# Kernel optimization log

Measured on AMD Instinct MI355X. Metric: run time of the kernel, lower is better.

Reference implementation:

```python
import jax, jax.numpy as jnp
import numpy as np

D = 1024  # d_model

def setup_inputs() -> dict:
    key = jax.random.key(0)
    ks = jax.random.split(key, 12)
    s = 1.0 / np.sqrt(D)  # torch Linear default init scale
    inp = {
        "q": jax.random.normal(ks[0], (4, 4096, D), dtype=jnp.float32),
        "k": jax.random.normal(ks[1], (4, 4096, D), dtype=jnp.float32),
        "v": jax.random.normal(ks[2], (4, 4096, D), dtype=jnp.float32),
        "Wq": jax.random.uniform(ks[3], (D, D), jnp.float32, -s, s),
        "bq": jax.random.uniform(ks[4], (D,), jnp.float32, -s, s),
        "Wk": jax.random.uniform(ks[5], (D, D), jnp.float32, -s, s),
        "bk": jax.random.uniform(ks[6], (D,), jnp.float32, -s, s),
        "Wv": jax.random.uniform(ks[7], (D, D), jnp.float32, -s, s),
        "bv": jax.random.uniform(ks[8], (D,), jnp.float32, -s, s),
        "Wo": jax.random.uniform(ks[9], (D, D), jnp.float32, -s, s),
        "bo": jax.random.uniform(ks[10], (D,), jnp.float32, -s, s),
    }
    return inp

def reference(q, k, v, Wq, bq, Wk, bk, Wv, bv, Wo, bo):
    # phi feature map: exp(-x^2 / 2)
    phi = lambda x: jnp.exp(-0.5 * x * x)
    Q = phi(q @ Wq.T + bq)            # [B, N, D]
    K = phi(k @ Wk.T + bk)            # [B, N, D]
    V = v @ Wv.T + bv                 # [B, N, D]
    # linear attention: aggregate K^T V once, then contract with Q
    KV = jnp.einsum('bnd,bnl->bdl', K, V)                 # [B, D, D]
    Z = 1.0 / (jnp.einsum('bnd,bd->bn', Q, K.sum(axis=1)) + 1e-6)  # [B, N]
    out = jnp.einsum('bnd,bdl->bnl', Q, KV) * Z[..., None]         # [B, N, D]
    return out @ Wo.T + bo
```

## Files before the change

kernel.cpp:

```cpp
#include <hip/hip_runtime.h>

typedef unsigned short u16;
typedef unsigned int u32;
typedef unsigned long long u64;

typedef __attribute__((ext_vector_type(8))) short short8;
typedef __attribute__((ext_vector_type(4))) float floatx4;

__device__ __forceinline__ float b2f(u16 h) {
  u32 u = ((u32)h) << 16;
  return __builtin_bit_cast(float, u);
}
__device__ __forceinline__ u16 f2b(float f) {
  u32 u = __builtin_bit_cast(u32, f);
  u32 r = 0x7FFFu + ((u >> 16) & 1u);
  return (u16)((u + r) >> 16);
}

__device__ __forceinline__ void gl_lds16(const void* g, void* l) {
  __builtin_amdgcn_global_load_lds(
      (__attribute__((address_space(1))) void*)(u64)g,
      (__attribute__((address_space(3))) void*)(u32)(u64)l, 16, 0, 0);
}

enum { EPI_PHI_BIAS = 0, EPI_BIAS = 1, EPI_NONE = 2,
       EPI_ZBIAS_F32 = 3 };

template<int EPI, bool TRANS_OUT>
__global__ __launch_bounds__(512, 2)
void gemm_bt256(const u16* __restrict__ Ap, const u16* __restrict__ Bp0,
                const float* __restrict__ bias, const float* __restrict__ Zall,
                void* __restrict__ Cp,
                int M, int N, int K, int ldA, int ldB, int ldC,
                long sAb, long sBb, long sCb, long sZb, int abmask, int kshift)
{
  constexpr int TSTRIDE = 65536;
  constexpr int BOFF    = 32768;
  __shared__ char smem[2 * TSTRIDE];

  const int tid  = threadIdx.x;
  const int lane = tid & 63;
  const int wave = tid >> 6;
  const int wm = wave >> 2, wn = wave & 3;
  const int fl = lane & 15;
  const int q  = lane >> 4;
  const int r4 = q * 4;
  const int bm0 = blockIdx.x * 256, bn0 = blockIdx.y * 256;
  const int bz = blockIdx.z;
  const int abz = bz & abmask;
  const int kbase = (bz >> kshift) * K;

  const u16* Ah = Ap  + (size_t)abz * sAb + kbase;
  const u16* Bh = Bp0 + (size_t)abz * sBb + kbase;

  const u16* gA[4]; const u16* gB[4]; int sL[4];
  #pragma unroll
  for (int n = 0; n < 4; ++n) {
    int j = n * 512 + tid;
    int R = j >> 3, c = (j & 7) ^ (R & 7);
    gA[n] = Ah + (size_t)(bm0 + R) * ldA + c * 8;
    gB[n] = Bh + (size_t)(bn0 + R) * ldB + c * 8;
    sL[n] = (n * 512 + wave * 64) * 16;
  }

  int aoff[8], boff[4];
  #pragma unroll
  for (int i = 0; i < 8; ++i) {
    int ra = wm * 128 + i * 16 + fl;
    aoff[i] = ra * 128 + ((q ^ (ra & 7)) * 16);
  }
  #pragma unroll
  for (int i = 0; i < 4; ++i) {
    int rb = wn * 64 + i * 16 + fl;
    boff[i] = rb * 128 + ((q ^ (rb & 7)) * 16);
  }

  floatx4 zero = {0.f, 0.f, 0.f, 0.f};
  floatx4 acc[8][4];
  #pragma unroll
  for (int i = 0; i < 8; ++i)
    #pragma unroll
    for (int j = 0; j < 4; ++j) acc[i][j] = zero;

  auto stage = [&](int t, char* base) {
    int k0 = t * 64;
    #pragma unroll
    for (int n = 0; n < 4; ++n) gl_lds16(gA[n] + k0, base + sL[n]);
    #pragma unroll
    for (int n = 0; n < 4; ++n) gl_lds16(gB[n] + k0, base + BOFF + sL[n]);
  };

  auto kstep = [&](const char* bufc, int xo) {
    short8 bF[4], aF[8];
    #pragma unroll
    for (int i = 0; i < 4; ++i) bF[i] = *(const short8*)(bufc + BOFF + (boff[i] ^ xo));
    #pragma unroll
    for (int i = 0; i < 8; ++i) aF[i] = *(const short8*)(bufc + (aoff[i] ^ xo));
    __builtin_amdgcn_s_setprio(1);
    #pragma unroll
    for (int mi = 0; mi < 8; ++mi)
      #pragma unroll
      for (int ni = 0; ni < 4; ++ni)
        acc[mi][ni] = __builtin_amdgcn_mfma_f32_16x16x32_bf16(
            aF[mi], bF[ni], acc[mi][ni], 0, 0, 0);
    __builtin_amdgcn_s_setprio(0);
  };

  const int NT = K >> 6;
  stage(0, smem);
  asm volatile("s_waitcnt vmcnt(0)\ns_barrier" ::: "memory");
  int cur = 0;
  for (int t = 0; t < NT; ++t) {
    if (t + 1 < NT) stage(t + 1, smem + (cur ^ TSTRIDE));
    const char* bufc = smem + cur;
    kstep(bufc, 0);
    kstep(bufc, 64);
    if (t + 1 < NT)
      asm volatile("s_waitcnt vmcnt(0) lgkmcnt(0)\ns_barrier" ::: "memory");
    cur ^= TSTRIDE;
  }

  if constexpr (!TRANS_OUT) {
    #pragma unroll
    for (int mi = 0; mi < 8; ++mi) {
      #pragma unroll
      for (int ni = 0; ni < 4; ++ni) {
        int col = bn0 + wn * 64 + ni * 16 + fl;
        #pragma unroll
        for (int r = 0; r < 4; ++r) {
          int row = bm0 + wm * 128 + mi * 16 + r4 + r;
          float vv = acc[mi][ni][r];
          if constexpr (EPI == EPI_PHI_BIAS) {
            vv += bias[col];
            vv = __expf(-0.5f * vv * vv);
          }
          if constexpr (EPI == EPI_ZBIAS_F32)
            vv = vv * Zall[(size_t)abz * sZb + row] + bias[col];
          if constexpr (EPI == EPI_ZBIAS_F32)
            ((float*)Cp)[(size_t)bz * sCb + (size_t)row * ldC + col] = vv;
          else
            ((u16*)Cp)[(size_t)bz * sCb + (size_t)row * ldC + col] = f2b(vv);
        }
      }
    }
  } else {
    u16* sT = (u16*)smem;
    #pragma unroll
    for (int p = 0; p < 2; ++p) {
      __syncthreads();
      if ((wn >> 1) == p) {
        #pragma unroll
        for (int mi = 0; mi < 8; ++mi) {
          #pragma unroll
          for (int ni = 0; ni < 4; ++ni) {
            int colL = wn * 64 + ni * 16 + fl;
            int row0 = wm * 128 + mi * 16 + r4;
            float bcol = bias[bn0 + colL];
            ushort4 h;
            #pragma unroll
            for (int r = 0; r < 4; ++r) {
              float vv = acc[mi][ni][r] + bcol;
              if constexpr (EPI == EPI_PHI_BIAS) vv = __expf(-0.5f * vv * vv);
              ((u16*)&h)[r] = f2b(vv);
            }
            *(ushort4*)(sT + (colL - p * 128) * 264 + row0) = h;
          }
        }
      }
      __syncthreads();
      #pragma unroll
      for (int i = 0; i < 8; ++i) {
        int c = tid + i * 512;
        int dloc = c >> 5, t8 = (c & 31) * 8;
        int4 vv = *(const int4*)(sT + dloc * 264 + t8);
        int gd = bn0 + p * 128 + dloc;
        int gt = bm0 + t8;
        int batch = gt >> 12, tt = gt & 4095;
        *(int4*)((u16*)Cp + ((size_t)batch * N + gd) * 4096 + tt) = vv;
      }
    }
  }
}

__global__ __launch_bounds__(256)
void fcvt(const float* __restrict__ src, u16* __restrict__ dst) {
  size_t i = ((size_t)blockIdx.x * 256 + threadIdx.x) * 8;
  float4 a = *(const float4*)(src + i);
  float4 b = *(const float4*)(src + i + 4);
  union { ushort4 h[2]; int4 v; } o;
  o.h[0].x = f2b(a.x); o.h[0].y = f2b(a.y); o.h[0].z = f2b(a.z); o.h[0].w = f2b(a.w);
  o.h[1].x = f2b(b.x); o.h[1].y = f2b(b.y); o.h[1].z = f2b(b.z); o.h[1].w = f2b(b.w);
  *(int4*)(dst + i) = o.v;
}

__global__ __launch_bounds__(256)
void wconv(const float* __restrict__ w0, const float* __restrict__ w1,
           const float* __restrict__ w2, const float* __restrict__ w3,
           u16* __restrict__ dst) {
  unsigned e = blockIdx.x * 256 + threadIdx.x;
  int mat = e >> 18;
  size_t off = (size_t)(e & 262143) * 4;
  const float* src = mat == 0 ? w0 : mat == 1 ? w1 : mat == 2 ? w2 : w3;
  float4 v = *(const float4*)(src + off);
  ushort4 h;
  h.x = f2b(v.x); h.y = f2b(v.y); h.z = f2b(v.z); h.w = f2b(v.w);
  *(ushort4*)(dst + (size_t)mat * 1048576 + off) = h;
}

__global__ __launch_bounds__(256)
void reduce4(const u16* __restrict__ P, u16* __restrict__ out) {
  size_t i = ((size_t)blockIdx.x * 256 + threadIdx.x) * 8;
  int4 a = *(const int4*)(P + i);
  int4 b = *(const int4*)(P + i + 4194304);
  int4 c = *(const int4*)(P + i + 8388608);
  int4 d = *(const int4*)(P + i + 12582912);
  const u16* ha = (const u16*)&a; const u16* hb = (const u16*)&b;
  const u16* hc = (const u16*)&c; const u16* hd = (const u16*)&d;
  ushort4 o0, o1;
  #pragma unroll
  for (int j = 0; j < 8; ++j) {
    float s = b2f(ha[j]) + b2f(hb[j]) + b2f(hc[j]) + b2f(hd[j]);
    ((u16*)(j < 4 ? &o0 : &o1))[j & 3] = f2b(s);
  }
  *(ushort4*)(out + i) = o0;
  *(ushort4*)(out + i + 4) = o1;
}

__global__ __launch_bounds__(256)
void ksum_rows(const u16* __restrict__ KT, float* __restrict__ Ksum) {
  int lane = threadIdx.x & 63;
  int row = blockIdx.x * 4 + (threadIdx.x >> 6);
  const u16* p = KT + (size_t)row * 4096;
  float s = 0.f;
  #pragma unroll
  for (int i = 0; i < 8; ++i) {
    int4 d = *(const int4*)(p + i * 512 + lane * 8);
    const u16* h = (const u16*)&d;
    #pragma unroll
    for (int j = 0; j < 8; ++j) s += b2f(h[j]);
  }
  #pragma unroll
  for (int off = 32; off; off >>= 1) s += __shfl_xor(s, off, 64);
  if (lane == 0) Ksum[row] = s;
}

__global__ __launch_bounds__(256)
void zden(const u16* __restrict__ Qb, const float* __restrict__ Ksum,
          float* __restrict__ Z) {
  int lane = threadIdx.x & 63;
  int t = blockIdx.x * 4 + (threadIdx.x >> 6);
  const u16* qp = Qb + (size_t)t * 1024;
  const float* ks = Ksum + (size_t)(t >> 12) * 1024;
  float s = 0.f;
  #pragma unroll
  for (int i = 0; i < 2; ++i) {
    int idx = i * 512 + lane * 8;
    int4 d = *(const int4*)(qp + idx);
    const u16* h = (const u16*)&d;
    float4 k0 = *(const float4*)(ks + idx);
    float4 k1 = *(const float4*)(ks + idx + 4);
    s += b2f(h[0]) * k0.x + b2f(h[1]) * k0.y + b2f(h[2]) * k0.z + b2f(h[3]) * k0.w
       + b2f(h[4]) * k1.x + b2f(h[5]) * k1.y + b2f(h[6]) * k1.z + b2f(h[7]) * k1.w;
  }
  #pragma unroll
  for (int off = 32; off; off >>= 1) s += __shfl_xor(s, off, 64);
  if (lane == 0) Z[t] = 1.0f / (s + 1e-6f);
}

extern "C" void kernel_launch(void* const* d_in, const int* in_sizes, int n_in,
                              void* d_out, int out_size, void* d_ws, size_t ws_size,
                              hipStream_t stream) {
  const float* q  = (const float*)d_in[0];
  const float* k  = (const float*)d_in[1];
  const float* v  = (const float*)d_in[2];
  const float* Wq = (const float*)d_in[3];
  const float* bq = (const float*)d_in[4];
  const float* Wk = (const float*)d_in[5];
  const float* bk = (const float*)d_in[6];
  const float* Wv = (const float*)d_in[7];
  const float* bv = (const float*)d_in[8];
  const float* Wo = (const float*)d_in[9];
  const float* bo = (const float*)d_in[10];
  float* out = (float*)d_out;

  u16* Wqb = (u16*)d_ws;
  u16* Wkb = Wqb + 1048576;
  u16* Wvb = Wkb + 1048576;
  u16* Wob = Wvb + 1048576;
  u16* Qb  = Wob + 1048576;
  u16* KT  = Qb  + 16777216;
  u16* VT  = KT  + 16777216;
  u16* KVr = VT  + 16777216;
  float* Ksum = (float*)(KVr + 4194304);
  float* Z    = Ksum + 4096;
  u16* kb16 = Qb;
  u16* vb16 = Qb;
  u16* Pkv  = Qb;
  u16* Pg   = VT;
  u16* Gp   = KT;
  u16* qb16 = VT;

  wconv<<<4096, 256, 0, stream>>>(Wq, Wk, Wv, Wo, Wqb);
  fcvt<<<8192, 256, 0, stream>>>(k, kb16);

  dim3 gp(64, 4, 1);
  gemm_bt256<EPI_PHI_BIAS, true><<<gp, 512, 0, stream>>>(
      kb16, Wkb, bk, nullptr, KT, 16384, 1024, 1024, 1024, 1024, 0,
      0, 0, 0, 0, 0, 2);
  ksum_rows<<<1024, 256, 0, stream>>>(KT, Ksum);

  fcvt<<<8192, 256, 0, stream>>>(v, vb16);
  gemm_bt256<EPI_BIAS, true><<<gp, 512, 0, stream>>>(
      vb16, Wvb, bv, nullptr, VT, 16384, 1024, 1024, 1024, 1024, 0,
      0, 0, 0, 0, 0, 2);

  dim3 g2(4, 4, 16);
  gemm_bt256<EPI_NONE, false><<<g2, 512, 0, stream>>>(
      KT, VT, nullptr, nullptr, Pkv, 1024, 1024, 1024, 4096, 4096, 1024,
      4194304L, 4194304L, 1048576L, 0, 3, 2);
  reduce4<<<2048, 256, 0, stream>>>(Pkv, KVr);

  dim3 gg(4, 4, 16);
  gemm_bt256<EPI_NONE, false><<<gg, 512, 0, stream>>>(
      Wob, KVr, nullptr, nullptr, Pg, 1024, 1024, 256, 1024, 1024, 1024,
      0L, 1048576L, 1048576L, 0, 3, 2);
  reduce4<<<2048, 256, 0, stream>>>(Pg, Gp);

  fcvt<<<8192, 256, 0, stream>>>(q, qb16);
  gemm_bt256<EPI_PHI_BIAS, false><<<gp, 512, 0, stream>>>(
      qb16, Wqb, bq, nullptr, Qb, 16384, 1024, 1024, 1024, 1024, 1024,
      0, 0, 0, 0, 0, 2);
  zden<<<4096, 256, 0, stream>>>(Qb, Ksum, Z);

  dim3 gf(16, 4, 4);
  gemm_bt256<EPI_ZBIAS_F32, false><<<gf, 512, 0, stream>>>(
      Qb, Gp, bo, Z, out, 4096, 1024, 1024, 1024, 1024, 1024,
      4194304L, 1048576L, 4194304L, 4096L, 3, 2);
}
```

Before: 301.2 us.

## Split GEMM k-loop into four quadrant phases interleaving LDS reads, prefetch, and MFMA

```diff
diff --git a/kernel.cpp b/kernel.cpp
--- a/kernel.cpp
+++ b/kernel.cpp
@@ -90,32 +90,101 @@
     for (int n = 0; n < 4; ++n) gl_lds16(gB[n] + k0, base + BOFF + sL[n]);
   };
 
-  auto kstep = [&](const char* bufc, int xo) {
-    short8 bF[4], aF[8];
-    #pragma unroll
-    for (int i = 0; i < 4; ++i) bF[i] = *(const short8*)(bufc + BOFF + (boff[i] ^ xo));
-    #pragma unroll
-    for (int i = 0; i < 8; ++i) aF[i] = *(const short8*)(bufc + (aoff[i] ^ xo));
-    __builtin_amdgcn_s_setprio(1);
-    #pragma unroll
-    for (int mi = 0; mi < 8; ++mi)
-      #pragma unroll
-      for (int ni = 0; ni < 4; ++ni)
-        acc[mi][ni] = __builtin_amdgcn_mfma_f32_16x16x32_bf16(
-            aF[mi], bF[ni], acc[mi][ni], 0, 0, 0);
-    __builtin_amdgcn_s_setprio(0);
-  };
-
   const int NT = K >> 6;
   stage(0, smem);
   asm volatile("s_waitcnt vmcnt(0)\ns_barrier" ::: "memory");
   int cur = 0;
   for (int t = 0; t < NT; ++t) {
-    if (t + 1 < NT) stage(t + 1, smem + (cur ^ TSTRIDE));
+    const bool pf = t + 1 < NT;
     const char* bufc = smem + cur;
-    kstep(bufc, 0);
-    kstep(bufc, 64);
-    if (t + 1 < NT)
+    char* stb = smem + (cur ^ TSTRIDE);
+    const int k1 = (t + 1) * 64;
+    short8 aL[8], aH[8], b01[4], b23[4];
+
+    #pragma unroll
+    for (int i = 0; i < 4; ++i) {
+      aL[2 * i]     = *(const short8*)(bufc + aoff[i]);
+      aL[2 * i + 1] = *(const short8*)(bufc + (aoff[i] ^ 64));
+    }
+    #pragma unroll
+    for (int i = 0; i < 2; ++i) {
+      b01[2 * i]     = *(const short8*)(bufc + BOFF + boff[i]);
+      b01[2 * i + 1] = *(const short8*)(bufc + BOFF + (boff[i] ^ 64));
+    }
+    if (pf) {
+      #pragma unroll
+      for (int n = 0; n < 4; ++n) gl_lds16(gA[n] + k1, stb + sL[n]);
+    }
+    __builtin_amdgcn_s_barrier();
+    asm volatile("s_waitcnt lgkmcnt(0)" ::: "memory");
+    __builtin_amdgcn_sched_barrier(0);
+    __builtin_amdgcn_s_setprio(1);
+    #pragma unroll
+    for (int kk = 0; kk < 2; ++kk)
+      #pragma unroll
+      for (int mi = 0; mi < 4; ++mi)
+        #pragma unroll
+        for (int ni = 0; ni < 2; ++ni)
+          acc[mi][ni] = __builtin_amdgcn_mfma_f32_16x16x32_bf16(
+              aL[2 * mi + kk], b01[2 * ni + kk], acc[mi][ni], 0, 0, 0);
+    __builtin_amdgcn_s_setprio(0);
+    __builtin_amdgcn_s_barrier();
+
+    #pragma unroll
+    for (int i = 0; i < 2; ++i) {
+      b23[2 * i]     = *(const short8*)(bufc + BOFF + boff[i + 2]);
+      b23[2 * i + 1] = *(const short8*)(bufc + BOFF + (boff[i + 2] ^ 64));
+    }
+    if (pf) {
+      #pragma unroll
+      for (int n = 0; n < 4; ++n) gl_lds16(gB[n] + k1, stb + BOFF + sL[n]);
+    }
+    __builtin_amdgcn_s_barrier();
+    asm volatile("s_waitcnt lgkmcnt(0)" ::: "memory");
+    __builtin_amdgcn_sched_barrier(0);
+    __builtin_amdgcn_s_setprio(1);
+    #pragma unroll
+    for (int kk = 0; kk < 2; ++kk)
+      #pragma unroll
+      for (int mi = 0; mi < 4; ++mi)
+        #pragma unroll
+        for (int ni = 0; ni < 2; ++ni)
+          acc[mi][ni + 2] = __builtin_amdgcn_mfma_f32_16x16x32_bf16(
+              aL[2 * mi + kk], b23[2 * ni + kk], acc[mi][ni + 2], 0, 0, 0);
+    __builtin_amdgcn_s_setprio(0);
+    __builtin_amdgcn_s_barrier();
+
+    #pragma unroll
+    for (int i = 0; i < 4; ++i) {
+      aH[2 * i]     = *(const short8*)(bufc + aoff[i + 4]);
+      aH[2 * i + 1] = *(const short8*)(bufc + (aoff[i + 4] ^ 64));
+    }
+    __builtin_amdgcn_s_barrier();
+    asm volatile("s_waitcnt lgkmcnt(0)" ::: "memory");
+    __builtin_amdgcn_sched_barrier(0);
+    __builtin_amdgcn_s_setprio(1);
+    #pragma unroll
+    for (int kk = 0; kk < 2; ++kk)
+      #pragma unroll
+      for (int mi = 0; mi < 4; ++mi)
+        #pragma unroll
+        for (int ni = 0; ni < 2; ++ni)
+          acc[mi + 4][ni + 2] = __builtin_amdgcn_mfma_f32_16x16x32_bf16(
+              aH[2 * mi + kk], b23[2 * ni + kk], acc[mi + 4][ni + 2], 0, 0, 0);
+    __builtin_amdgcn_s_setprio(0);
+    __builtin_amdgcn_s_barrier();
+
+    __builtin_amdgcn_s_setprio(1);
+    #pragma unroll
+    for (int kk = 0; kk < 2; ++kk)
+      #pragma unroll
+      for (int mi = 0; mi < 4; ++mi)
+        #pragma unroll
+        for (int ni = 0; ni < 2; ++ni)
+          acc[mi + 4][ni] = __builtin_amdgcn_mfma_f32_16x16x32_bf16(
+              aH[2 * mi + kk], b01[2 * ni + kk], acc[mi + 4][ni], 0, 0, 0);
+    __builtin_amdgcn_s_setprio(0);
+    if (pf)
       asm volatile("s_waitcnt vmcnt(0) lgkmcnt(0)\ns_barrier" ::: "memory");
     cur ^= TSTRIDE;
   }
```

Measured after the change: 304.3 us. No clear change (+1.0%).

## Fuse fp32-to-bf16 activation conversion into projection GEMM A-tile loads

Applied to the files above, without the earlier changes.

```diff
diff --git a/kernel.cpp b/kernel.cpp
--- a/kernel.cpp
+++ b/kernel.cpp
@@ -26,9 +26,9 @@
 enum { EPI_PHI_BIAS = 0, EPI_BIAS = 1, EPI_NONE = 2,
        EPI_ZBIAS_F32 = 3 };
 
-template<int EPI, bool TRANS_OUT>
+template<int EPI, bool TRANS_OUT, bool A_F32>
 __global__ __launch_bounds__(512, 2)
-void gemm_bt256(const u16* __restrict__ Ap, const u16* __restrict__ Bp0,
+void gemm_bt256(const void* __restrict__ Ap, const u16* __restrict__ Bp0,
                 const float* __restrict__ bias, const float* __restrict__ Zall,
                 void* __restrict__ Cp,
                 int M, int N, int K, int ldA, int ldB, int ldC,
@@ -50,17 +50,20 @@
   const int abz = bz & abmask;
   const int kbase = (bz >> kshift) * K;
 
-  const u16* Ah = Ap  + (size_t)abz * sAb + kbase;
-  const u16* Bh = Bp0 + (size_t)abz * sBb + kbase;
-
-  const u16* gA[4]; const u16* gB[4]; int sL[4];
+  const u16*   Ah = (const u16*)Ap   + (size_t)abz * sAb + kbase;
+  const float* Af = (const float*)Ap + (size_t)abz * sAb + kbase;
+  const u16*   Bh = Bp0 + (size_t)abz * sBb + kbase;
+
+  const u16* gA[4]; const float* gAf[4]; const u16* gB[4]; int sL[4], dL[4];
   #pragma unroll
   for (int n = 0; n < 4; ++n) {
     int j = n * 512 + tid;
     int R = j >> 3, c = (j & 7) ^ (R & 7);
-    gA[n] = Ah + (size_t)(bm0 + R) * ldA + c * 8;
+    if constexpr (A_F32) gAf[n] = Af + (size_t)(bm0 + R) * ldA + c * 8;
+    else                 gA[n]  = Ah + (size_t)(bm0 + R) * ldA + c * 8;
     gB[n] = Bh + (size_t)(bn0 + R) * ldB + c * 8;
     sL[n] = (n * 512 + wave * 64) * 16;
+    dL[n] = j * 16;
   }
 
   int aoff[8], boff[4];
@@ -82,12 +85,35 @@
     #pragma unroll
     for (int j = 0; j < 4; ++j) acc[i][j] = zero;
 
-  auto stage = [&](int t, char* base) {
-    int k0 = t * 64;
-    #pragma unroll
-    for (int n = 0; n < 4; ++n) gl_lds16(gA[n] + k0, base + sL[n]);
-    #pragma unroll
-    for (int n = 0; n < 4; ++n) gl_lds16(gB[n] + k0, base + BOFF + sL[n]);
+  auto stageB = [&](int t, char* base) {
+    #pragma unroll
+    for (int n = 0; n < 4; ++n) gl_lds16(gB[n] + t * 64, base + BOFF + sL[n]);
+  };
+  auto stageA_dma = [&](int t, char* base) {
+    #pragma unroll
+    for (int n = 0; n < 4; ++n) gl_lds16(gA[n] + t * 64, base + sL[n]);
+  };
+
+  float4 rA[8];
+  auto loadA = [&](int t) {
+    #pragma unroll
+    for (int n = 0; n < 4; ++n) {
+      rA[2 * n]     = *(const float4*)(gAf[n] + t * 64);
+      rA[2 * n + 1] = *(const float4*)(gAf[n] + t * 64 + 4);
+    }
+  };
+  auto packA = [&](char* base) {
+    #pragma unroll
+    for (int n = 0; n < 4; ++n) {
+      const u32* xb = (const u32*)&rA[2 * n];
+      const u32* yb = (const u32*)&rA[2 * n + 1];
+      union { u32 w[4]; short8 s; } cv;
+      cv.w[0] = __builtin_amdgcn_perm(xb[1], xb[0], 0x07060302u);
+      cv.w[1] = __builtin_amdgcn_perm(xb[3], xb[2], 0x07060302u);
+      cv.w[2] = __builtin_amdgcn_perm(yb[1], yb[0], 0x07060302u);
+      cv.w[3] = __builtin_amdgcn_perm(yb[3], yb[2], 0x07060302u);
+      *(short8*)(base + dL[n]) = cv.s;
+    }
   };
 
   auto kstep = [&](const char* bufc, int xo) {
@@ -107,17 +133,40 @@
   };
 
   const int NT = K >> 6;
-  stage(0, smem);
-  asm volatile("s_waitcnt vmcnt(0)\ns_barrier" ::: "memory");
-  int cur = 0;
-  for (int t = 0; t < NT; ++t) {
-    if (t + 1 < NT) stage(t + 1, smem + (cur ^ TSTRIDE));
-    const char* bufc = smem + cur;
-    kstep(bufc, 0);
-    kstep(bufc, 64);
-    if (t + 1 < NT)
-      asm volatile("s_waitcnt vmcnt(0) lgkmcnt(0)\ns_barrier" ::: "memory");
-    cur ^= TSTRIDE;
+  if constexpr (A_F32) {
+    loadA(0); stageB(0, smem);
+    asm volatile("s_waitcnt vmcnt(4)" ::: "memory");
+    packA(smem);
+    asm volatile("s_waitcnt vmcnt(0) lgkmcnt(0)\ns_barrier" ::: "memory");
+    int cur = 0;
+    for (int t = 0; t < NT; ++t) {
+      const bool pf = t + 1 < NT;
+      const char* bufc = smem + cur;
+      char* bufn = smem + (cur ^ TSTRIDE);
+      if (pf) { loadA(t + 1); stageB(t + 1, bufn); }
+      kstep(bufc, 0);
+      if (pf) packA(bufn);
+      kstep(bufc, 64);
+      if (pf)
+        asm volatile("s_waitcnt vmcnt(0) lgkmcnt(0)\ns_barrier" ::: "memory");
+      cur ^= TSTRIDE;
+    }
+  } else {
+    stageA_dma(0, smem); stageB(0, smem);
+    asm volatile("s_waitcnt vmcnt(0)\ns_barrier" ::: "memory");
+    int cur = 0;
+    for (int t = 0; t < NT; ++t) {
+      if (t + 1 < NT) {
+        stageA_dma(t + 1, smem + (cur ^ TSTRIDE));
+        stageB(t + 1, smem + (cur ^ TSTRIDE));
+      }
+      const char* bufc = smem + cur;
+      kstep(bufc, 0);
+      kstep(bufc, 64);
+      if (t + 1 < NT)
+        asm volatile("s_waitcnt vmcnt(0) lgkmcnt(0)\ns_barrier" ::: "memory");
+      cur ^= TSTRIDE;
+    }
   }
 
   if constexpr (!TRANS_OUT) {
@@ -183,17 +232,6 @@
 }
 
 __global__ __launch_bounds__(256)
-void fcvt(const float* __restrict__ src, u16* __restrict__ dst) {
-  size_t i = ((size_t)blockIdx.x * 256 + threadIdx.x) * 8;
-  float4 a = *(const float4*)(src + i);
-  float4 b = *(const float4*)(src + i + 4);
-  union { ushort4 h[2]; int4 v; } o;
-  o.h[0].x = f2b(a.x); o.h[0].y = f2b(a.y); o.h[0].z = f2b(a.z); o.h[0].w = f2b(a.w);
-  o.h[1].x = f2b(b.x); o.h[1].y = f2b(b.y); o.h[1].z = f2b(b.z); o.h[1].w = f2b(b.w);
-  *(int4*)(dst + i) = o.v;
-}
-
-__global__ __launch_bounds__(256)
 void wconv(const float* __restrict__ w0, const float* __restrict__ w1,
            const float* __restrict__ w2, const float* __restrict__ w3,
            u16* __restrict__ dst) {
@@ -293,47 +331,41 @@
   u16* KVr = VT  + 16777216;
   float* Ksum = (float*)(KVr + 4194304);
   float* Z    = Ksum + 4096;
-  u16* kb16 = Qb;
-  u16* vb16 = Qb;
-  u16* Pkv  = Qb;
-  u16* Pg   = VT;
-  u16* Gp   = KT;
-  u16* qb16 = VT;
+  u16* Pkv = Qb;
+  u16* Pg  = VT;
+  u16* Gp  = KT;
 
   wconv<<<4096, 256, 0, stream>>>(Wq, Wk, Wv, Wo, Wqb);
-  fcvt<<<8192, 256, 0, stream>>>(k, kb16);
 
   dim3 gp(64, 4, 1);
-  gemm_bt256<EPI_PHI_BIAS, true><<<gp, 512, 0, stream>>>(
-      kb16, Wkb, bk, nullptr, KT, 16384, 1024, 1024, 1024, 1024, 0,
+  gemm_bt256<EPI_PHI_BIAS, true, true><<<gp, 512, 0, stream>>>(
+      k, Wkb, bk, nullptr, KT, 16384, 1024, 1024, 1024, 1024, 0,
       0, 0, 0, 0, 0, 2);
   ksum_rows<<<1024, 256, 0, stream>>>(KT, Ksum);
 
-  fcvt<<<8192, 256, 0, stream>>>(v, vb16);
-  gemm_bt256<EPI_BIAS, true><<<gp, 512, 0, stream>>>(
-      vb16, Wvb, bv, nullptr, VT, 16384, 1024, 1024, 1024, 1024, 0,
+  gemm_bt256<EPI_BIAS, true, true><<<gp, 512, 0, stream>>>(
+      v, Wvb, bv, nullptr, VT, 16384, 1024, 1024, 1024, 1024, 0,
       0, 0, 0, 0, 0, 2);
 
   dim3 g2(4, 4, 16);
-  gemm_bt256<EPI_NONE, false><<<g2, 512, 0, stream>>>(
+  gemm_bt256<EPI_NONE, false, false><<<g2, 512, 0, stream>>>(
       KT, VT, nullptr, nullptr, Pkv, 1024, 1024, 1024, 4096, 4096, 1024,
       4194304L, 4194304L, 1048576L, 0, 3, 2);
   reduce4<<<2048, 256, 0, stream>>>(Pkv, KVr);
 
   dim3 gg(4, 4, 16);
-  gemm_bt256<EPI_NONE, false><<<gg, 512, 0, stream>>>(
+  gemm_bt256<EPI_NONE, false, false><<<gg, 512, 0, stream>>>(
       Wob, KVr, nullptr, nullptr, Pg, 1024, 1024, 256, 1024, 1024, 1024,
       0L, 1048576L, 1048576L, 0, 3, 2);
   reduce4<<<2048, 256, 0, stream>>>(Pg, Gp);
 
-  fcvt<<<8192, 256, 0, stream>>>(q, qb16);
-  gemm_bt256<EPI_PHI_BIAS, false><<<gp, 512, 0, stream>>>(
-      qb16, Wqb, bq, nullptr, Qb, 16384, 1024, 1024, 1024, 1024, 1024,
+  gemm_bt256<EPI_PHI_BIAS, false, true><<<gp, 512, 0, stream>>>(
+      q, Wqb, bq, nullptr, Qb, 16384, 1024, 1024, 1024, 1024, 1024,
       0, 0, 0, 0, 0, 2);
   zden<<<4096, 256, 0, stream>>>(Qb, Ksum, Z);
 
   dim3 gf(16, 4, 4);
-  gemm_bt256<EPI_ZBIAS_F32, false><<<gf, 512, 0, stream>>>(
+  gemm_bt256<EPI_ZBIAS_F32, false, false><<<gf, 512, 0, stream>>>(
       Qb, Gp, bo, Z, out, 4096, 1024, 1024, 1024, 1024, 1024,
       4194304L, 1048576L, 4194304L, 4096L, 3, 2);
 }
```

Result: faster. 289.2 us (-4.0%).
